# Optimization experiments

Hardware: AMD Instinct MI355X
Metric: run time of the kernel (lower is better)

Reference implementation:

```python
import jax, jax.numpy as jnp
import numpy as np

N, IN_DIM, OUT_DIM, HEADS = 3072, 512, 64, 8
EDGE_PROB = 0.01
NEG_SLOPE = 0.2


def setup_inputs() -> dict:
    key = jax.random.key(0)
    k1, k2, k3, k4, k5 = jax.random.split(key, 5)
    x = jax.random.normal(k1, (N, IN_DIM), dtype=jnp.float32)
    # sparse-ish dense adjacency mask with self-loops
    adj = (jax.random.uniform(k2, (N, N)) < EDGE_PROB).astype(jnp.float32)
    adj = jnp.maximum(adj, jnp.eye(N, dtype=jnp.float32))
    W = jax.random.normal(k3, (HEADS, IN_DIM, OUT_DIM), dtype=jnp.float32) * 0.1
    a_src = jax.random.normal(k4, (HEADS, OUT_DIM), dtype=jnp.float32) * 0.1
    a_dst = jax.random.normal(k5, (HEADS, OUT_DIM), dtype=jnp.float32) * 0.1
    return {"x": x, "adj": adj, "W": W, "a_src": a_src, "a_dst": a_dst}


def reference(x, adj, W, a_src, a_dst):
    # per-head linear projection: [H, N, OUT]
    h = jnp.einsum("ni,hio->hno", x, W)
    # attention logits e_ij = LeakyReLU(a_src . h_i + a_dst . h_j)
    f_src = jnp.einsum("hno,ho->hn", h, a_src)  # [H, N]
    f_dst = jnp.einsum("hno,ho->hn", h, a_dst)  # [H, N]
    e = f_src[:, :, None] + f_dst[:, None, :]   # [H, N, N]
    e = jax.nn.leaky_relu(e, negative_slope=NEG_SLOPE)
    # mask non-edges, row-softmax over neighbors
    e = jnp.where(adj[None] > 0, e, jnp.float32(-1e9))
    att = jax.nn.softmax(e, axis=-1)             # [H, N, N]
    # aggregate neighbor features per head
    out = jnp.einsum("hij,hjo->hio", att, h)     # [H, N, OUT]
    # concat heads along feature dim -> [N, H*OUT]
    return out.transpose(1, 0, 2).reshape(N, HEADS * OUT_DIM)
```

## Files before the change

kernel.cpp:

```cpp
#include <hip/hip_runtime.h>

#define N_NODES 3072
#define IN_DIM 512
#define OUT_DIM 64
#define HEADS 8
#define NEG_SLOPE 0.2f
#define MAX_E 128

typedef __attribute__((ext_vector_type(8))) short bf16x8;
typedef __attribute__((ext_vector_type(4))) float f32x4;

#define XFRAG_TILES (N_NODES / 16)
#define KTILES (IN_DIM / 32)
#define XFRAG_THREADS (XFRAG_TILES * KTILES * 64)
#define WFRAG_THREADS (HEADS * KTILES * 4 * 64)

__device__ inline unsigned short f2bf(float f) {
    union { float f; unsigned u; } v; v.f = f;
    unsigned r = (v.u + 0x7FFF + ((v.u >> 16) & 1)) >> 16;
    return (unsigned short)r;
}

__device__ inline float waveAllMax(float v) {
#pragma unroll
    for (int o = 32; o; o >>= 1) v = fmaxf(v, __shfl_xor(v, o, 64));
    return v;
}
__device__ inline float waveAllSum(float v) {
#pragma unroll
    for (int o = 32; o; o >>= 1) v += __shfl_xor(v, o, 64);
    return v;
}

__global__ __launch_bounds__(256) void gat_prep(
    const float* __restrict__ x, const float* __restrict__ W,
    short* __restrict__ xfrag, short* __restrict__ wfrag) {
    int tid = blockIdx.x * 256 + threadIdx.x;
    if (tid < XFRAG_THREADS) {
        int lane = tid & 63;
        int kt = (tid >> 6) & (KTILES - 1);
        int rt = tid >> 10;
        int m = rt * 16 + (lane & 15);
        int k0 = kt * 32 + (lane >> 4) * 8;
        const float4* xp = (const float4*)(x + (size_t)m * IN_DIM + k0);
        float4 v0 = xp[0], v1 = xp[1];
        bf16x8 r;
        r[0] = (short)f2bf(v0.x); r[1] = (short)f2bf(v0.y);
        r[2] = (short)f2bf(v0.z); r[3] = (short)f2bf(v0.w);
        r[4] = (short)f2bf(v1.x); r[5] = (short)f2bf(v1.y);
        r[6] = (short)f2bf(v1.z); r[7] = (short)f2bf(v1.w);
        ((bf16x8*)xfrag)[tid] = r;
    } else {
        int t2 = tid - XFRAG_THREADS;
        if (t2 >= WFRAG_THREADS) return;
        int lane = t2 & 63;
        int c = (t2 >> 6) & 3;
        int kt = (t2 >> 8) & (KTILES - 1);
        int head = t2 >> 12;
        int n = c * 16 + (lane & 15);
        int k0 = kt * 32 + (lane >> 4) * 8;
        const float* wp = W + ((size_t)head * IN_DIM + k0) * OUT_DIM + n;
        bf16x8 r;
#pragma unroll
        for (int j = 0; j < 8; ++j) r[j] = (short)f2bf(wp[(size_t)j * OUT_DIM]);
        ((bf16x8*)wfrag)[t2] = r;
    }
}

__global__ __launch_bounds__(256) void gat_proj(
    const short* __restrict__ xfrag, const short* __restrict__ wfrag,
    const float* __restrict__ a_src, const float* __restrict__ a_dst,
    float* __restrict__ hbuf, float* __restrict__ fsrc, float* __restrict__ fdst) {
    __shared__ float hs[32][OUT_DIM + 1];

    const int t = threadIdx.x;
    const int lane = t & 63;
    const int w = t >> 6;
    const int head = blockIdx.y;
    const int m0 = blockIdx.x * 32;
    const int rt0 = blockIdx.x * 2;

    const bf16x8* xa = (const bf16x8*)xfrag + (size_t)rt0 * 16 * 64 + lane;
    const bf16x8* wb = (const bf16x8*)wfrag + ((size_t)head * KTILES * 4 + w) * 64 + lane;

    f32x4 acc0 = {0.f, 0.f, 0.f, 0.f};
    f32x4 acc1 = {0.f, 0.f, 0.f, 0.f};
#pragma unroll
    for (int kt = 0; kt < KTILES; ++kt) {
        bf16x8 a0 = xa[kt * 64];
        bf16x8 a1 = xa[(16 + kt) * 64];
        bf16x8 b  = wb[kt * 4 * 64];
        acc0 = __builtin_amdgcn_mfma_f32_16x16x32_bf16(a0, b, acc0, 0, 0, 0);
        acc1 = __builtin_amdgcn_mfma_f32_16x16x32_bf16(a1, b, acc1, 0, 0, 0);
    }

    const int col = w * 16 + (lane & 15);
    const int r0 = (lane >> 4) * 4;
    float* gp = hbuf + ((size_t)head * N_NODES + m0) * OUT_DIM;
#pragma unroll
    for (int i2 = 0; i2 < 4; ++i2) {
        hs[r0 + i2][col] = acc0[i2];
        hs[r0 + 16 + i2][col] = acc1[i2];
        gp[(size_t)(r0 + i2) * OUT_DIM + col] = acc0[i2];
        gp[(size_t)(r0 + 16 + i2) * OUT_DIM + col] = acc1[i2];
    }
    __syncthreads();

    {
        const float* av = (t < 128 ? a_src : a_dst) + head * OUT_DIM;
        const int tt = t & 127;
        const int row = tt >> 2, part = tt & 3;
        float s = 0.f;
#pragma unroll
        for (int n = 0; n < 16; ++n) s += hs[row][part * 16 + n] * av[part * 16 + n];
        s += __shfl_xor(s, 1, 64);
        s += __shfl_xor(s, 2, 64);
        if (part == 0) {
            float* dst = (t < 128 ? fsrc : fdst);
            dst[head * N_NODES + m0 + row] = s;
        }
    }
}

__global__ __launch_bounds__(256) void gat_agg(
    const float* __restrict__ adj, const float* __restrict__ hbuf,
    const float* __restrict__ fsrc, const float* __restrict__ fdst,
    float* __restrict__ out) {
    __shared__ int s_idx[MAX_E];
    __shared__ float s_pe[4][2][2 * MAX_E];
    __shared__ int s_cnt;

    const int i = blockIdx.x;
    const int t = threadIdx.x;
    if (t == 0) s_cnt = 0;
    __syncthreads();

    const float4* arow4 = (const float4*)(adj + (size_t)i * N_NODES);
#pragma unroll
    for (int it = 0; it < 3; ++it) {
        const int jj = t + it * 256;
        float4 v = arow4[jj];
        const int j = jj * 4;
        if (v.x > 0.f) { int s = atomicAdd(&s_cnt, 1); if (s < MAX_E) s_idx[s] = j; }
        if (v.y > 0.f) { int s = atomicAdd(&s_cnt, 1); if (s < MAX_E) s_idx[s] = j + 1; }
        if (v.z > 0.f) { int s = atomicAdd(&s_cnt, 1); if (s < MAX_E) s_idx[s] = j + 2; }
        if (v.w > 0.f) { int s = atomicAdd(&s_cnt, 1); if (s < MAX_E) s_idx[s] = j + 3; }
    }
    __syncthreads();
    const int E = min(s_cnt, MAX_E);
    const int w = t >> 6;
    const int lane = t & 63;
    const int h0 = w, h1 = w + 4;

    const float fiA = fsrc[h0 * N_NODES + i];
    const float fiB = fsrc[h1 * N_NODES + i];

    float mA = -1e30f, mB = -1e30f;
    for (int k = lane; k < E; k += 64) {
        int j = s_idx[k];
        float eA = fiA + fdst[h0 * N_NODES + j];
        float eB = fiB + fdst[h1 * N_NODES + j];
        eA = eA > 0.f ? eA : NEG_SLOPE * eA;
        eB = eB > 0.f ? eB : NEG_SLOPE * eB;
        s_pe[w][0][2 * k] = eA; s_pe[w][0][2 * k + 1] = __int_as_float(j);
        s_pe[w][1][2 * k] = eB; s_pe[w][1][2 * k + 1] = __int_as_float(j);
        mA = fmaxf(mA, eA); mB = fmaxf(mB, eB);
    }
    mA = waveAllMax(mA); mB = waveAllMax(mB);

    float sA = 0.f, sB = 0.f;
    for (int k = lane; k < E; k += 64) {
        float pA = __expf(s_pe[w][0][2 * k] - mA); s_pe[w][0][2 * k] = pA; sA += pA;
        float pB = __expf(s_pe[w][1][2 * k] - mB); s_pe[w][1][2 * k] = pB; sB += pB;
    }
    sA = waveAllSum(sA); sB = waveAllSum(sB);
    const float invA = 1.f / sA, invB = 1.f / sB;

    float accA = 0.f, accB = 0.f;
#pragma unroll 8
    for (int k = 0; k < E; ++k) {
        float2 a = *(const float2*)&s_pe[w][0][2 * k];
        float2 b = *(const float2*)&s_pe[w][1][2 * k];
        int ja = __float_as_int(a.y), jb = __float_as_int(b.y);
        accA = fmaf(a.x, hbuf[((size_t)h0 * N_NODES + ja) * OUT_DIM + lane], accA);
        accB = fmaf(b.x, hbuf[((size_t)h1 * N_NODES + jb) * OUT_DIM + lane], accB);
    }
    out[(size_t)i * (HEADS * OUT_DIM) + h0 * OUT_DIM + lane] = accA * invA;
    out[(size_t)i * (HEADS * OUT_DIM) + h1 * OUT_DIM + lane] = accB * invB;
}

extern "C" void kernel_launch(void* const* d_in, const int* in_sizes, int n_in,
                              void* d_out, int out_size, void* d_ws, size_t ws_size,
                              hipStream_t stream) {
    const float* x     = (const float*)d_in[0];
    const float* adj   = (const float*)d_in[1];
    const float* W     = (const float*)d_in[2];
    const float* a_src = (const float*)d_in[3];
    const float* a_dst = (const float*)d_in[4];
    float* out = (float*)d_out;

    float* hbuf = (float*)d_ws;
    float* fsrc = hbuf + (size_t)HEADS * N_NODES * OUT_DIM;
    float* fdst = fsrc + HEADS * N_NODES;
    short* xfrag = (short*)(fdst + HEADS * N_NODES);
    short* wfrag = xfrag + (size_t)XFRAG_TILES * KTILES * 64 * 8;

    gat_prep<<<(XFRAG_THREADS + WFRAG_THREADS) / 256, 256, 0, stream>>>(
        x, W, xfrag, wfrag);
    gat_proj<<<dim3(N_NODES / 32, HEADS), 256, 0, stream>>>(
        xfrag, wfrag, a_src, a_dst, hbuf, fsrc, fdst);
    gat_agg<<<N_NODES, 256, 0, stream>>>(adj, hbuf, fsrc, fdst, out);
}
```

Measured before the change: 114.9 us.

## Store projected features as node-major bf16 and gather two columns per lane

The projection kernel now writes h as bf16 in a node-major [N, H*OUT] layout instead of fp32 head-major. The aggregation kernel splits each wave into two half-waves, one per head, and each lane loads a packed pair of bf16 values. This halves gather traffic and places all heads of a neighbor in one contiguous row. In exchange it adds bf16 rounding to the aggregated features and uses strided 2-byte stores in the projection kernel.

```diff
diff --git a/kernel.cpp b/kernel.cpp
--- a/kernel.cpp
+++ b/kernel.cpp
@@ -19,17 +19,6 @@
     union { float f; unsigned u; } v; v.f = f;
     unsigned r = (v.u + 0x7FFF + ((v.u >> 16) & 1)) >> 16;
     return (unsigned short)r;
-}
-
-__device__ inline float waveAllMax(float v) {
-#pragma unroll
-    for (int o = 32; o; o >>= 1) v = fmaxf(v, __shfl_xor(v, o, 64));
-    return v;
-}
-__device__ inline float waveAllSum(float v) {
-#pragma unroll
-    for (int o = 32; o; o >>= 1) v += __shfl_xor(v, o, 64);
-    return v;
 }
 
 __global__ __launch_bounds__(256) void gat_prep(
@@ -70,7 +59,7 @@
 __global__ __launch_bounds__(256) void gat_proj(
     const short* __restrict__ xfrag, const short* __restrict__ wfrag,
     const float* __restrict__ a_src, const float* __restrict__ a_dst,
-    float* __restrict__ hbuf, float* __restrict__ fsrc, float* __restrict__ fdst) {
+    unsigned short* __restrict__ hb, float* __restrict__ fsrc, float* __restrict__ fdst) {
     __shared__ float hs[32][OUT_DIM + 1];
 
     const int t = threadIdx.x;
@@ -96,13 +85,13 @@
 
     const int col = w * 16 + (lane & 15);
     const int r0 = (lane >> 4) * 4;
-    float* gp = hbuf + ((size_t)head * N_NODES + m0) * OUT_DIM;
+    unsigned short* hp = hb + (size_t)m0 * (HEADS * OUT_DIM) + head * OUT_DIM + col;
 #pragma unroll
     for (int i2 = 0; i2 < 4; ++i2) {
         hs[r0 + i2][col] = acc0[i2];
         hs[r0 + 16 + i2][col] = acc1[i2];
-        gp[(size_t)(r0 + i2) * OUT_DIM + col] = acc0[i2];
-        gp[(size_t)(r0 + 16 + i2) * OUT_DIM + col] = acc1[i2];
+        hp[(size_t)(r0 + i2) * (HEADS * OUT_DIM)] = f2bf(acc0[i2]);
+        hp[(size_t)(r0 + 16 + i2) * (HEADS * OUT_DIM)] = f2bf(acc1[i2]);
     }
     __syncthreads();
 
@@ -123,11 +112,11 @@
 }
 
 __global__ __launch_bounds__(256) void gat_agg(
-    const float* __restrict__ adj, const float* __restrict__ hbuf,
+    const float* __restrict__ adj, const unsigned short* __restrict__ hb,
     const float* __restrict__ fsrc, const float* __restrict__ fdst,
     float* __restrict__ out) {
     __shared__ int s_idx[MAX_E];
-    __shared__ float s_pe[4][2][2 * MAX_E];
+    __shared__ float s_p[HEADS][MAX_E];
     __shared__ int s_cnt;
 
     const int i = blockIdx.x;
@@ -148,45 +137,47 @@
     }
     __syncthreads();
     const int E = min(s_cnt, MAX_E);
+
     const int w = t >> 6;
     const int lane = t & 63;
-    const int h0 = w, h1 = w + 4;
-
-    const float fiA = fsrc[h0 * N_NODES + i];
-    const float fiB = fsrc[h1 * N_NODES + i];
-
-    float mA = -1e30f, mB = -1e30f;
-    for (int k = lane; k < E; k += 64) {
-        int j = s_idx[k];
-        float eA = fiA + fdst[h0 * N_NODES + j];
-        float eB = fiB + fdst[h1 * N_NODES + j];
-        eA = eA > 0.f ? eA : NEG_SLOPE * eA;
-        eB = eB > 0.f ? eB : NEG_SLOPE * eB;
-        s_pe[w][0][2 * k] = eA; s_pe[w][0][2 * k + 1] = __int_as_float(j);
-        s_pe[w][1][2 * k] = eB; s_pe[w][1][2 * k + 1] = __int_as_float(j);
-        mA = fmaxf(mA, eA); mB = fmaxf(mB, eB);
-    }
-    mA = waveAllMax(mA); mB = waveAllMax(mB);
-
-    float sA = 0.f, sB = 0.f;
-    for (int k = lane; k < E; k += 64) {
-        float pA = __expf(s_pe[w][0][2 * k] - mA); s_pe[w][0][2 * k] = pA; sA += pA;
-        float pB = __expf(s_pe[w][1][2 * k] - mB); s_pe[w][1][2 * k] = pB; sB += pB;
-    }
-    sA = waveAllSum(sA); sB = waveAllSum(sB);
-    const float invA = 1.f / sA, invB = 1.f / sB;
-
-    float accA = 0.f, accB = 0.f;
+    const int half = lane >> 5;
+    const int sl = lane & 31;
+    const int head = 2 * w + half;
+
+    const float fi = fsrc[head * N_NODES + i];
+
+    float m = -1e30f;
+    for (int k = sl; k < E; k += 32) {
+        float e = fi + fdst[head * N_NODES + s_idx[k]];
+        e = e > 0.f ? e : NEG_SLOPE * e;
+        s_p[head][k] = e;
+        m = fmaxf(m, e);
+    }
+#pragma unroll
+    for (int o = 16; o; o >>= 1) m = fmaxf(m, __shfl_xor(m, o, 64));
+
+    float sum = 0.f;
+    for (int k = sl; k < E; k += 32) {
+        float p = __expf(s_p[head][k] - m);
+        s_p[head][k] = p;
+        sum += p;
+    }
+#pragma unroll
+    for (int o = 16; o; o >>= 1) sum += __shfl_xor(sum, o, 64);
+    const float inv = 1.f / sum;
+
+    const unsigned short* hbase = hb + head * OUT_DIM + sl * 2;
+    float a0 = 0.f, a1 = 0.f;
 #pragma unroll 8
     for (int k = 0; k < E; ++k) {
-        float2 a = *(const float2*)&s_pe[w][0][2 * k];
-        float2 b = *(const float2*)&s_pe[w][1][2 * k];
-        int ja = __float_as_int(a.y), jb = __float_as_int(b.y);
-        accA = fmaf(a.x, hbuf[((size_t)h0 * N_NODES + ja) * OUT_DIM + lane], accA);
-        accB = fmaf(b.x, hbuf[((size_t)h1 * N_NODES + jb) * OUT_DIM + lane], accB);
-    }
-    out[(size_t)i * (HEADS * OUT_DIM) + h0 * OUT_DIM + lane] = accA * invA;
-    out[(size_t)i * (HEADS * OUT_DIM) + h1 * OUT_DIM + lane] = accB * invB;
+        const int j = s_idx[k];
+        const float p = s_p[head][k];
+        const unsigned u = *(const unsigned*)(hbase + (size_t)j * (HEADS * OUT_DIM));
+        a0 = fmaf(p, __uint_as_float(u << 16), a0);
+        a1 = fmaf(p, __uint_as_float(u & 0xffff0000u), a1);
+    }
+    float2 r = {a0 * inv, a1 * inv};
+    *(float2*)(out + (size_t)i * (HEADS * OUT_DIM) + head * OUT_DIM + sl * 2) = r;
 }
 
 extern "C" void kernel_launch(void* const* d_in, const int* in_sizes, int n_in,
@@ -199,15 +190,15 @@
     const float* a_dst = (const float*)d_in[4];
     float* out = (float*)d_out;
 
-    float* hbuf = (float*)d_ws;
-    float* fsrc = hbuf + (size_t)HEADS * N_NODES * OUT_DIM;
+    float* fsrc = (float*)d_ws;
     float* fdst = fsrc + HEADS * N_NODES;
-    short* xfrag = (short*)(fdst + HEADS * N_NODES);
+    unsigned short* hb = (unsigned short*)(fdst + HEADS * N_NODES);
+    short* xfrag = (short*)(hb + (size_t)N_NODES * HEADS * OUT_DIM);
     short* wfrag = xfrag + (size_t)XFRAG_TILES * KTILES * 64 * 8;
 
     gat_prep<<<(XFRAG_THREADS + WFRAG_THREADS) / 256, 256, 0, stream>>>(
         x, W, xfrag, wfrag);
     gat_proj<<<dim3(N_NODES / 32, HEADS), 256, 0, stream>>>(
-        xfrag, wfrag, a_src, a_dst, hbuf, fsrc, fdst);
-    gat_agg<<<N_NODES, 256, 0, stream>>>(adj, hbuf, fsrc, fdst, out);
-}
+        xfrag, wfrag, a_src, a_dst, hb, fsrc, fdst);
+    gat_agg<<<N_NODES, 256, 0, stream>>>(adj, hb, fsrc, fdst, out);
+}
```

Result: faster. 107.9 us (-6.1%).
